# Optimization experiments

Hardware: AMD Instinct MI355X
Metric: run time of the kernel (lower is better)

The kernel has to match this reference:

```python
import jax, jax.numpy as jnp
import numpy as np
from jax import lax

B, LATENT, SEQ, HID, OUT = 4096, 128, 512, 32, 64


def setup_inputs() -> dict:
    key = jax.random.key(0)
    ks = jax.random.split(key, 9)
    s = 1.0 / np.sqrt(HID)  # PyTorch-style init scale
    f32 = jnp.float32
    return {
        "z": jax.random.normal(ks[0], (B, LATENT), f32),
        "init_W": jax.random.uniform(ks[1], (HID, LATENT), f32, -s, s),
        "init_b": jax.random.uniform(ks[2], (HID,), f32, -s, s),
        "W_ih": jax.random.uniform(ks[3], (4 * HID, HID), f32, -s, s),
        "W_hh": jax.random.uniform(ks[4], (4 * HID, HID), f32, -s, s),
        "b_ih": jax.random.uniform(ks[5], (4 * HID,), f32, -s, s),
        "b_hh": jax.random.uniform(ks[6], (4 * HID,), f32, -s, s),
        "out_W": jax.random.uniform(ks[7], (OUT, HID), f32, -s, s),
        "out_b": jax.random.uniform(ks[8], (OUT,), f32, -s, s),
    }


def reference(z, init_W, init_b, W_ih, W_hh, b_ih, b_hh, out_W, out_b):
    # init_fc: z -> h0 (num_layers=1); cell starts at zero
    h0 = z @ init_W.T + init_b  # [B, H]
    c0 = jnp.zeros_like(h0)

    # x_in is all zeros, so the input-to-hidden term is a constant bias;
    # compute it once (keeps W_ih in the graph, matmul with zeros == 0).
    x_zero = jnp.zeros((z.shape[0], W_ih.shape[1]), z.dtype)
    gate_const = x_zero @ W_ih.T + b_ih + b_hh  # [B, 4H]

    def step(carry, _):
        h, c = carry
        gates = h @ W_hh.T + gate_const  # [B, 4H], PyTorch gate order i,f,g,o
        i, f, g, o = jnp.split(gates, 4, axis=-1)
        i = jax.nn.sigmoid(i)
        f = jax.nn.sigmoid(f)
        g = jnp.tanh(g)
        o = jax.nn.sigmoid(o)
        c = f * c + i * g
        h = o * jnp.tanh(c)
        return (h, c), h

    _, hs = lax.scan(step, (h0, c0), None, length=SEQ)  # [T, B, H]
    out = jnp.transpose(hs, (1, 0, 2))  # [B, T, H] (batch_first)
    y = out @ out_W.T + out_b  # [B, T, OUT]
    return y
```

## Files before the change

### kernel.cpp

```cpp
#include <hip/hip_runtime.h>


#define B_SZ   4096
#define LATENT 128
#define SEQ    512
#define HID    32
#define OUT_N  64
#define ROWS   16
#define LSW    40

typedef _Float16 f16x8 __attribute__((ext_vector_type(8)));
typedef _Float16 f16x4 __attribute__((ext_vector_type(4)));
typedef float    f32x4 __attribute__((ext_vector_type(4)));

__device__ __forceinline__ float fexp2(float x) { return __builtin_amdgcn_exp2f(x); }
__device__ __forceinline__ float frcp(float x)  { return __builtin_amdgcn_rcpf(x); }
__device__ __forceinline__ float sigm(float x) {
    return frcp(1.f + fexp2(-1.44269504088896341f * x));
}
__device__ __forceinline__ float tanh_f(float x) {
    return fmaf(-2.f, frcp(1.f + fexp2(2.88539008177792681f * x)), 1.f);
}
__device__ __forceinline__ void lds_barrier() {
    asm volatile("s_waitcnt lgkmcnt(0)\n\ts_barrier" ::: "memory");
}

__global__ __launch_bounds__(256)
void lstm_tr4(const float* __restrict__ z,
              const float* __restrict__ init_W,
              const float* __restrict__ init_b,
              const float* __restrict__ W_hh,
              const float* __restrict__ b_ih,
              const float* __restrict__ b_hh,
              const float* __restrict__ out_W,
              const float* __restrict__ out_b,
              float* __restrict__ y)
{
    __shared__ __align__(16) _Float16 hst[ROWS * LSW];
    __shared__ unsigned int hx[2][4][64];

    const int tid  = threadIdx.x;
    const int w    = tid >> 6;
    const int lane = tid & 63;
    const int n_   = lane & 15;
    const int kb   = lane >> 4;
    const int jj   = w >> 1;
    const int p2   = w & 1;
    const int rbase = blockIdx.x * ROWS;

    f16x8 wf[4];
    f32x4 bacc[4];
#pragma unroll
    for (int m = 0; m < 4; m++) {
        int g = 2 * m + jj;
        const float* row = W_hh + (size_t)(16 * g + n_) * HID;
        f16x8 v;
#pragma unroll
        for (int rr = 0; rr < 4; rr++) {
            v[rr]     = (_Float16)row[4 * kb + rr];
            v[4 + rr] = (_Float16)row[4 * kb + 16 + rr];
        }
        wf[m] = v;
        f32x4 b;
#pragma unroll
        for (int r = 0; r < 4; r++) {
            int G = 16 * g + 4 * kb + r;
            b[r] = b_ih[G] + b_hh[G];
        }
        bacc[m] = b;
    }
    f16x8 owf;
    f32x4 oacc;
    {
        const float* row = out_W + (size_t)(16 * w + n_) * HID;
        f16x8 v;
#pragma unroll
        for (int rr = 0; rr < 4; rr++) {
            v[rr]     = (_Float16)row[4 * kb + rr];
            v[4 + rr] = (_Float16)row[4 * kb + 16 + rr];
        }
        owf = v;
#pragma unroll
        for (int r = 0; r < 4; r++) oacc[r] = out_b[16 * w + 4 * kb + r];
    }

#pragma unroll
    for (int i = 0; i < 2; i++) {
        int e = tid + 256 * i;
        int m = e >> 5, j = e & 31;
        const float4* zp = (const float4*)(z + (size_t)(rbase + m) * LATENT);
        const float4* wp = (const float4*)(init_W + (size_t)j * LATENT);
        float acc = init_b[j];
#pragma unroll
        for (int k = 0; k < LATENT / 4; k++) {
            float4 a4 = zp[k], b4 = wp[k];
            acc = fmaf(a4.x, b4.x, acc); acc = fmaf(a4.y, b4.y, acc);
            acc = fmaf(a4.z, b4.z, acc); acc = fmaf(a4.w, b4.w, acc);
        }
        hst[m * LSW + j] = (_Float16)acc;
    }
    __syncthreads();

    f16x8 a;
    {
        f16x4 lo = *(const f16x4*)&hst[n_ * LSW + 4 * kb];
        f16x4 hi = *(const f16x4*)&hst[n_ * LSW + 4 * kb + 16];
#pragma unroll
        for (int r = 0; r < 4; r++) { a[r] = lo[r]; a[4 + r] = hi[r]; }
    }

    float c2[2] = {0.f, 0.f};

    float* yb = y + (size_t)(rbase + n_) * SEQ * OUT_N + 16 * w + 4 * kb;

    for (int t = 0; t < SEQ; t += 2) {
#pragma unroll
        for (int u = 0; u < 2; u++) {
            f32x4 acc[4];
#pragma unroll
            for (int m = 0; m < 4; m++)
                acc[m] = __builtin_amdgcn_mfma_f32_16x16x32_f16(wf[m], a, bacc[m], 0, 0, 0);

            unsigned int pk;
            {
                _Float16 hh[2];
#pragma unroll
                for (int r2 = 0; r2 < 2; r2++) {
                    int r = 2 * p2 + r2;
                    float gi = sigm(acc[0][r]);
                    float gf = sigm(acc[1][r]);
                    float gg = tanh_f(acc[2][r]);
                    float go = sigm(acc[3][r]);
                    float cn = fmaf(gf, c2[r2], gi * gg);
                    c2[r2] = cn;
                    hh[r2] = (_Float16)(go * tanh_f(cn));
                }
                union { _Float16 h[2]; unsigned int u32; } cv;
                cv.h[0] = hh[0]; cv.h[1] = hh[1];
                pk = cv.u32;
            }
            hx[u][w][lane] = pk;
            lds_barrier();

            union { f16x8 v; unsigned int u32[4]; } nv;
#pragma unroll
            for (int q = 0; q < 4; q++) nv.u32[q] = hx[u][q][lane];
            a = nv.v;

            f32x4 py = __builtin_amdgcn_mfma_f32_16x16x32_f16(owf, a, oacc, 0, 0, 0);
            *(f32x4*)(yb + (size_t)(t + u) * OUT_N) = py;
        }
    }
}

extern "C" void kernel_launch(void* const* d_in, const int* in_sizes, int n_in,
                              void* d_out, int out_size, void* d_ws, size_t ws_size,
                              hipStream_t stream) {
    const float* z      = (const float*)d_in[0];
    const float* init_W = (const float*)d_in[1];
    const float* init_b = (const float*)d_in[2];
    const float* W_hh   = (const float*)d_in[4];
    const float* b_ih   = (const float*)d_in[5];
    const float* b_hh   = (const float*)d_in[6];
    const float* out_W  = (const float*)d_in[7];
    const float* out_b  = (const float*)d_in[8];
    float* yout = (float*)d_out;

    lstm_tr4<<<B_SZ / ROWS, 256, 0, stream>>>(z, init_W, init_b, W_hh, b_ih, b_hh,
                                              out_W, out_b, yout);
}
```

Measured before the change: 666.4 us.

## Split LSTM gate work across eight waves per block

Doubles the block to 512 threads so each wave handles one accumulator row instead of two. This halves the serial transcendental work per wave on each recurrent step. Every wave still issues the same four gate MFMAs, so that matrix work is duplicated. Hidden-state exchange now goes through a reshaped 16-bit LDS buffer, and only half the waves compute and store the output projection. The cost is more waves synchronizing at each per-step barrier and redundant MFMA issue.

```diff
diff --git a/kernel.cpp b/kernel.cpp
--- a/kernel.cpp
+++ b/kernel.cpp
@@ -25,8 +25,8 @@
     asm volatile("s_waitcnt lgkmcnt(0)\n\ts_barrier" ::: "memory");
 }
 
-__global__ __launch_bounds__(256)
-void lstm_tr4(const float* __restrict__ z,
+__global__ __launch_bounds__(512)
+void lstm_tr8(const float* __restrict__ z,
               const float* __restrict__ init_W,
               const float* __restrict__ init_b,
               const float* __restrict__ W_hh,
@@ -37,15 +37,15 @@
               float* __restrict__ y)
 {
     __shared__ __align__(16) _Float16 hst[ROWS * LSW];
-    __shared__ unsigned int hx[2][4][64];
+    __shared__ __align__(8) unsigned short hx[2][2][64][4];
 
     const int tid  = threadIdx.x;
     const int w    = tid >> 6;
     const int lane = tid & 63;
     const int n_   = lane & 15;
     const int kb   = lane >> 4;
-    const int jj   = w >> 1;
-    const int p2   = w & 1;
+    const int jj   = w & 1;
+    const int r_   = w >> 1;
     const int rbase = blockIdx.x * ROWS;
 
     f16x8 wf[4];
@@ -72,7 +72,8 @@
     f16x8 owf;
     f32x4 oacc;
     {
-        const float* row = out_W + (size_t)(16 * w + n_) * HID;
+        int p = r_;
+        const float* row = out_W + (size_t)(16 * p + n_) * HID;
         f16x8 v;
 #pragma unroll
         for (int rr = 0; rr < 4; rr++) {
@@ -81,13 +82,11 @@
         }
         owf = v;
 #pragma unroll
-        for (int r = 0; r < 4; r++) oacc[r] = out_b[16 * w + 4 * kb + r];
+        for (int r = 0; r < 4; r++) oacc[r] = out_b[16 * p + 4 * kb + r];
     }
 
-#pragma unroll
-    for (int i = 0; i < 2; i++) {
-        int e = tid + 256 * i;
-        int m = e >> 5, j = e & 31;
+    {
+        int m = tid >> 5, j = tid & 31;
         const float4* zp = (const float4*)(z + (size_t)(rbase + m) * LATENT);
         const float4* wp = (const float4*)(init_W + (size_t)j * LATENT);
         float acc = init_b[j];
@@ -109,46 +108,41 @@
         for (int r = 0; r < 4; r++) { a[r] = lo[r]; a[4 + r] = hi[r]; }
     }
 
-    float c2[2] = {0.f, 0.f};
+    float c1 = 0.f;
 
-    float* yb = y + (size_t)(rbase + n_) * SEQ * OUT_N + 16 * w + 4 * kb;
+    float* yb = y + (size_t)(rbase + n_) * SEQ * OUT_N + 16 * r_ + 4 * kb;
 
-    for (int t = 0; t < SEQ; t += 2) {
+    for (int t = 0; t < SEQ; t += 4) {
 #pragma unroll
-        for (int u = 0; u < 2; u++) {
+        for (int u = 0; u < 4; u++) {
+            const int par = u & 1;
             f32x4 acc[4];
 #pragma unroll
             for (int m = 0; m < 4; m++)
                 acc[m] = __builtin_amdgcn_mfma_f32_16x16x32_f16(wf[m], a, bacc[m], 0, 0, 0);
 
-            unsigned int pk;
             {
-                _Float16 hh[2];
-#pragma unroll
-                for (int r2 = 0; r2 < 2; r2++) {
-                    int r = 2 * p2 + r2;
-                    float gi = sigm(acc[0][r]);
-                    float gf = sigm(acc[1][r]);
-                    float gg = tanh_f(acc[2][r]);
-                    float go = sigm(acc[3][r]);
-                    float cn = fmaf(gf, c2[r2], gi * gg);
-                    c2[r2] = cn;
-                    hh[r2] = (_Float16)(go * tanh_f(cn));
-                }
-                union { _Float16 h[2]; unsigned int u32; } cv;
-                cv.h[0] = hh[0]; cv.h[1] = hh[1];
-                pk = cv.u32;
+                float gi = sigm(acc[0][r_]);
+                float gf = sigm(acc[1][r_]);
+                float gg = tanh_f(acc[2][r_]);
+                float go = sigm(acc[3][r_]);
+                float cn = fmaf(gf, c1, gi * gg);
+                c1 = cn;
+                union { _Float16 h; unsigned short u16; } cv;
+                cv.h = (_Float16)(go * tanh_f(cn));
+                hx[par][jj][lane][r_] = cv.u16;
             }
-            hx[u][w][lane] = pk;
             lds_barrier();
 
-            union { f16x8 v; unsigned int u32[4]; } nv;
+            f16x4 lo = *(const f16x4*)&hx[par][0][lane][0];
+            f16x4 hi = *(const f16x4*)&hx[par][1][lane][0];
 #pragma unroll
-            for (int q = 0; q < 4; q++) nv.u32[q] = hx[u][q][lane];
-            a = nv.v;
+            for (int r = 0; r < 4; r++) { a[r] = lo[r]; a[4 + r] = hi[r]; }
 
-            f32x4 py = __builtin_amdgcn_mfma_f32_16x16x32_f16(owf, a, oacc, 0, 0, 0);
-            *(f32x4*)(yb + (size_t)(t + u) * OUT_N) = py;
+            if (jj == 0) {
+                f32x4 py = __builtin_amdgcn_mfma_f32_16x16x32_f16(owf, a, oacc, 0, 0, 0);
+                *(f32x4*)(yb + (size_t)(t + u) * OUT_N) = py;
+            }
         }
     }
 }
@@ -166,6 +160,6 @@
     const float* out_b  = (const float*)d_in[8];
     float* yout = (float*)d_out;
 
-    lstm_tr4<<<B_SZ / ROWS, 256, 0, stream>>>(z, init_W, init_b, W_hh, b_ih, b_hh,
+    lstm_tr8<<<B_SZ / ROWS, 512, 0, stream>>>(z, init_W, init_b, W_hh, b_ih, b_hh,
                                               out_W, out_b, yout);
 }
```

Measured after the change: 635.3 us. 4.7% less time.
